# Kernel optimization log

Hardware: AMD Instinct MI355X
Metric: run time of the kernel (lower is better)

Reference implementation:

```python
import jax, jax.numpy as jnp
import numpy as np

B_COEF = 0.1          # position-offset scale 'b'
STRIDE = (1, 1)
PADDING = (1, 1)


def setup_inputs() -> dict:
    key = jax.random.key(0)
    k1, k2, k3 = jax.random.split(key, 3)
    x = jax.random.normal(k1, (16, 64, 128, 128), dtype=jnp.float32)
    kernel = jax.random.normal(k2, (128, 64, 3, 3), dtype=jnp.float32)
    bias = jax.random.normal(k3, (128,), dtype=jnp.float32)
    return {"x": x, "kernel": kernel, "bias": bias}


def _conv(inp, w):
    pads = [(PADDING[0], PADDING[0]), (PADDING[1], PADDING[1])]
    return jax.lax.conv_general_dilated(
        inp, w, window_strides=STRIDE, padding=pads,
        dimension_numbers=("NCHW", "OIHW", "NCHW"))


def reference(x, kernel, bias):
    # out[b,o,p] = sum_i x_unf[b,i,p] * (kernel_flat[o,i] + b*grid[p]) + bias[o]
    # = conv(x, kernel) + b*grid[p] * sum_i x_unf[b,i,p] + bias  (rank-1 separable)
    kh, kw = kernel.shape[2], kernel.shape[3]
    main = _conv(x, kernel)                                  # (B, O, Ho, Wo)
    H_out, W_out = main.shape[2], main.shape[3]

    # sum over in_channels and kernel window = ones-conv of channel-summed input
    ones_k = jnp.ones((1, 1, kh, kw), dtype=x.dtype)
    patch_sum = _conv(x.sum(axis=1, keepdims=True), ones_k)  # (B, 1, Ho, Wo)

    # Replicate torch meshgrid(arange(W_out), arange(H_out), indexing='ij')
    # -> flatten (W,H) row-major -> consumed as (H,W) row-major by the view.
    gx = jnp.arange(W_out)[:, None] + jnp.arange(H_out)[None, :]  # (Wo, Ho)
    grid2d = gx.reshape(-1).reshape(H_out, W_out).astype(x.dtype)  # (Ho, Wo)

    return main + B_COEF * grid2d * patch_sum + bias[None, :, None, None]
```

## Files before the change

### kernel.cpp

```cpp
#include <hip/hip_runtime.h>
#include <hip/hip_bf16.h>


typedef __attribute__((ext_vector_type(8))) short short8;
typedef __attribute__((ext_vector_type(4))) float f32x4;

#define B_COEF 0.1f
constexpr int CI = 64, CO = 128, H = 128, W = 128;
constexpr int XPAD = 72;

static __device__ inline short bf16s(float v) {
    __hip_bfloat16 b = __float2bfloat16(v);
    return *reinterpret_cast<short*>(&b);
}


__global__ __launch_bounds__(256)
void prep_x(const float* __restrict__ x, __hip_bfloat16* __restrict__ xt,
            float* __restrict__ S) {
    __shared__ float tile[64 * 129];
    __shared__ float ssum[256];
    const int h = blockIdx.x, b = blockIdx.y, tid = threadIdx.x;
    const int w = tid & 127, cip = tid >> 7;

    float sacc = 0.0f;
    for (int it = 0; it < 32; ++it) {
        int ci = it * 2 + cip;
        float v = x[(((size_t)b * CI + ci) * H + h) * W + w];
        tile[ci * 129 + w] = v;
        sacc += v;
    }
    ssum[tid] = sacc;
    __syncthreads();
    if (tid < 128)
        S[((size_t)b * H + h) * W + tid] = ssum[tid] + ssum[tid + 128];

    const int c8 = (tid & 7) * 8, wl = tid >> 3;
#pragma unroll
    for (int it = 0; it < 4; ++it) {
        int ww = wl + it * 32;
        short8 pk;
#pragma unroll
        for (int j = 0; j < 8; ++j)
            pk[j] = bf16s(tile[(c8 + j) * 129 + ww]);
        *(short8*)(xt + (((size_t)b * H + h) * W + ww) * CI + c8) = pk;
    }
}

__global__ void prep_wq(const float* __restrict__ wgt, __hip_bfloat16* __restrict__ wq) {
    int idx = blockIdx.x * 256 + threadIdx.x;
    if (idx < 9 * CO * CI) {
        int tap = idx >> 13;
        int rem = idx & 8191;
        int oc = rem >> 6, ci = rem & 63;
        int kc = ci >> 5, j = ci & 31;
        wq[(((tap * 2 + kc) * CO + oc) << 5) + j] =
            __float2bfloat16(wgt[(oc * CI + ci) * 9 + tap]);
    }
}

__global__ __launch_bounds__(256, 2)
void conv_main(const __hip_bfloat16* __restrict__ xt,
               const __hip_bfloat16* __restrict__ wq,
               const float* __restrict__ S,
               const float* __restrict__ bias,
               float* __restrict__ out) {
    __shared__ __hip_bfloat16 xrow[3][130 * XPAD];
    __shared__ float ssum[132];

    const int tid = threadIdx.x, h = blockIdx.x, b = blockIdx.y;
    const int lane = tid & 63, waveid = tid >> 6;
    const int lo16 = lane & 15, quad = lane >> 4;
    const int m0 = (waveid & 1) * 64, n0 = (waveid >> 1) * 64;

    const int c8 = (tid & 7) * 8, wl = tid >> 3;
#pragma unroll
    for (int r = 0; r < 3; ++r) {
        const int gh = h - 1 + r;
#pragma unroll
        for (int it = 0; it < 5; ++it) {
            int w = wl + it * 32;
            if (w < 130) {
                int gw = w - 1;
                short8 v = {0, 0, 0, 0, 0, 0, 0, 0};
                if (gh >= 0 && gh < H && gw >= 0 && gw < W)
                    v = *(const short8*)(xt + (((size_t)b * H + gh) * W + gw) * CI + c8);
                *(short8*)&xrow[r][w * XPAD + c8] = v;
            }
        }
    }
    if (tid < 130) {
        int gw = tid - 1;
        float s = 0.0f;
        if (gw >= 0 && gw < W) {
#pragma unroll
            for (int r = 0; r < 3; ++r) {
                int gh = h - 1 + r;
                if (gh >= 0 && gh < H) s += S[((size_t)b * H + gh) * W + gw];
            }
        }
        ssum[tid] = s;
    }
    __syncthreads();

    f32x4 acc[4][4] = {};

#pragma unroll
    for (int kh = 0; kh < 3; ++kh) {
#pragma unroll
        for (int kw = 0; kw < 3; ++kw) {
            const int tap = kh * 3 + kw;
            short8 bq[2][4];
#pragma unroll
            for (int kc = 0; kc < 2; ++kc)
#pragma unroll
                for (int ni = 0; ni < 4; ++ni)
                    bq[kc][ni] = *(const short8*)(
                        wq + (((tap * 2 + kc) * CO + n0 + ni * 16 + lo16) << 5) + quad * 8);
#pragma unroll
            for (int kc = 0; kc < 2; ++kc) {
                short8 af[4];
#pragma unroll
                for (int mi = 0; mi < 4; ++mi)
                    af[mi] = *(const short8*)
                        &xrow[kh][(m0 + mi * 16 + lo16 + kw) * XPAD + kc * 32 + quad * 8];
#pragma unroll
                for (int mi = 0; mi < 4; ++mi)
#pragma unroll
                    for (int ni = 0; ni < 4; ++ni)
                        acc[mi][ni] = __builtin_amdgcn_mfma_f32_16x16x32_bf16(
                            af[mi], bq[kc][ni], acc[mi][ni], 0, 0, 0);
            }
        }
    }

#pragma unroll
    for (int mi = 0; mi < 4; ++mi) {
        const int wbase = m0 + mi * 16 + quad * 4;
        float cs[6];
#pragma unroll
        for (int r = 0; r < 6; ++r) cs[r] = ssum[wbase + r];
        float ps[4], cf[4];
#pragma unroll
        for (int r = 0; r < 4; ++r) {
            ps[r] = cs[r] + cs[r + 1] + cs[r + 2];
            cf[r] = B_COEF * (float)(h + wbase + r);
        }
#pragma unroll
        for (int ni = 0; ni < 4; ++ni) {
            const int oc = n0 + ni * 16 + lo16;
            const float bv = bias[oc];
            f32x4 v = acc[mi][ni];
#pragma unroll
            for (int r = 0; r < 4; ++r) v[r] = v[r] + cf[r] * ps[r] + bv;
            *(f32x4*)(out + (((size_t)b * CO + oc) * H + h) * W + wbase) = v;
        }
    }
}


constexpr int WPAD = 72;

__global__ void prep_w_fb(const float* __restrict__ wgt, __hip_bfloat16* __restrict__ wt) {
    int idx = blockIdx.x * 256 + threadIdx.x;
    if (idx < 9 * CO * CI) {
        int tap = idx / (CO * CI);
        int rem = idx - tap * (CO * CI);
        int oc = rem >> 6, ci = rem & 63;
        wt[idx] = __float2bfloat16(wgt[(oc * CI + ci) * 9 + tap]);
    }
}

__global__ __launch_bounds__(256, 2)
void conv_fb(const float* __restrict__ x, const __hip_bfloat16* __restrict__ wt,
             const float* __restrict__ bias, float* __restrict__ out) {
    __shared__ __hip_bfloat16 xrow[130 * XPAD];
    __shared__ __hip_bfloat16 wlds[CO * WPAD];
    __shared__ float colsum[132];

    const int tid = threadIdx.x;
    const int h = blockIdx.x, b = blockIdx.y;
    const int lane = tid & 63, waveid = tid >> 6;
    const int lo16 = lane & 15, quad = lane >> 4;
    const int m0 = (waveid & 1) * 64, n0 = (waveid >> 1) * 64;

    f32x4 acc[4][4] = {};
    if (tid < 132) colsum[tid] = 0.0f;
    const float* xb = x + (size_t)b * CI * H * W;

    const int w16 = tid & 15, cipl = (tid >> 4) & 3, rest0 = tid >> 6;

    for (int kh = 0; kh < 3; ++kh) {
        const int gh = h - 1 + kh;
        __syncthreads();
        for (int it = 0; it < 18; ++it) {
            int rest = rest0 + it * 4;
            int whi = rest % 9, ciph = rest / 9;
            int w = whi * 16 + w16;
            int ci0 = (ciph * 4 + cipl) * 2;
            int gw = w - 1;
            float x0 = 0.0f, x1 = 0.0f;
            if (w < 130 && gw >= 0 && gw < W && gh >= 0 && gh < H) {
                const float* p = xb + (size_t)ci0 * (H * W) + gh * W + gw;
                x0 = p[0];
                x1 = p[H * W];
            }
            if (w < 130) {
                __hip_bfloat162 pk;
                pk.x = __float2bfloat16(x0);
                pk.y = __float2bfloat16(x1);
                *(__hip_bfloat162*)&xrow[w * XPAD + ci0] = pk;
            }
            float cs = x0 + x1;
            cs += __shfl_xor(cs, 16);
            cs += __shfl_xor(cs, 32);
            if (quad == 0 && w < 130) atomicAdd(&colsum[w], cs);
        }
        for (int kw = 0; kw < 3; ++kw) {
            __syncthreads();
            {
                const __hip_bfloat16* wtap = wt + (kh * 3 + kw) * (CO * CI);
#pragma unroll
                for (int it = 0; it < 4; ++it) {
                    int j = tid + it * 256;
                    int oc = j >> 3, ch = (j & 7) * 8;
                    short8 v = *(const short8*)(wtap + oc * CI + ch);
                    *(short8*)&wlds[oc * WPAD + ch] = v;
                }
            }
            __syncthreads();
#pragma unroll
            for (int kc = 0; kc < 2; ++kc) {
                const int krow = kc * 32 + quad * 8;
                short8 af[4], bf[4];
#pragma unroll
                for (int mi = 0; mi < 4; ++mi)
                    af[mi] = *(const short8*)&xrow[(m0 + mi * 16 + lo16 + kw) * XPAD + krow];
#pragma unroll
                for (int ni = 0; ni < 4; ++ni)
                    bf[ni] = *(const short8*)&wlds[(n0 + ni * 16 + lo16) * WPAD + krow];
#pragma unroll
                for (int mi = 0; mi < 4; ++mi)
#pragma unroll
                    for (int ni = 0; ni < 4; ++ni)
                        acc[mi][ni] = __builtin_amdgcn_mfma_f32_16x16x32_bf16(
                            af[mi], bf[ni], acc[mi][ni], 0, 0, 0);
            }
        }
    }
    __syncthreads();
#pragma unroll
    for (int mi = 0; mi < 4; ++mi) {
        const int wbase = m0 + mi * 16 + quad * 4;
        float cs[6];
#pragma unroll
        for (int r = 0; r < 6; ++r) cs[r] = colsum[wbase + r];
        float ps[4], cf[4];
#pragma unroll
        for (int r = 0; r < 4; ++r) {
            ps[r] = cs[r] + cs[r + 1] + cs[r + 2];
            cf[r] = B_COEF * (float)(h + wbase + r);
        }
#pragma unroll
        for (int ni = 0; ni < 4; ++ni) {
            const int oc = n0 + ni * 16 + lo16;
            const float bv = bias[oc];
            f32x4 v = acc[mi][ni];
#pragma unroll
            for (int r = 0; r < 4; ++r) v[r] = v[r] + cf[r] * ps[r] + bv;
            *(f32x4*)(out + (((size_t)b * CO + oc) * H + h) * W + wbase) = v;
        }
    }
}


extern "C" void kernel_launch(void* const* d_in, const int* in_sizes, int n_in,
                              void* d_out, int out_size, void* d_ws, size_t ws_size,
                              hipStream_t stream) {
    const float* x    = (const float*)d_in[0];
    const float* wgt  = (const float*)d_in[1];
    const float* bias = (const float*)d_in[2];
    float* out = (float*)d_out;

    const size_t XT_BYTES = (size_t)16 * H * W * CI * 2;
    const size_t S_BYTES  = (size_t)16 * H * W * 4;
    const size_t WQ_BYTES = (size_t)9 * 2 * CO * 32 * 2;

    if (ws_size >= XT_BYTES + S_BYTES + WQ_BYTES) {
        __hip_bfloat16* xt = (__hip_bfloat16*)d_ws;
        float* S           = (float*)((char*)d_ws + XT_BYTES);
        __hip_bfloat16* wq = (__hip_bfloat16*)((char*)d_ws + XT_BYTES + S_BYTES);
        prep_x<<<dim3(H, 16), dim3(256), 0, stream>>>(x, xt, S);
        prep_wq<<<dim3(288), dim3(256), 0, stream>>>(wgt, wq);
        conv_main<<<dim3(H, 16), dim3(256), 0, stream>>>(xt, wq, S, bias, out);
    } else {
        __hip_bfloat16* wt = (__hip_bfloat16*)d_ws;
        prep_w_fb<<<dim3(288), dim3(256), 0, stream>>>(wgt, wt);
        conv_fb<<<dim3(H, 16), dim3(256), 0, stream>>>(x, wt, bias, out);
    }
}
```

Before: 249.3 us.

## Compute two output rows per conv block and vectorize prep_x transpose

conv_main now computes two output rows per block. It loads four input rows into shared memory and reuses each weight fragment across both rows, which halves the grid and the redundant halo-row and weight loads. prep_x now does 128-bit vector global loads, uses an XOR-swizzled shared tile to avoid bank conflicts, and reduces channel sums through eight partial buffers. Both kernels remap blockIdx to row indices, likely to spread work across XCDs or cache. The larger accumulator array doubles register pressure and may reduce occupancy or cause spills.

```diff
diff --git a/kernel.cpp b/kernel.cpp
--- a/kernel.cpp
+++ b/kernel.cpp
@@ -18,31 +18,43 @@
 __global__ __launch_bounds__(256)
 void prep_x(const float* __restrict__ x, __hip_bfloat16* __restrict__ xt,
             float* __restrict__ S) {
-    __shared__ float tile[64 * 129];
-    __shared__ float ssum[256];
-    const int h = blockIdx.x, b = blockIdx.y, tid = threadIdx.x;
-    const int w = tid & 127, cip = tid >> 7;
-
-    float sacc = 0.0f;
-    for (int it = 0; it < 32; ++it) {
-        int ci = it * 2 + cip;
-        float v = x[(((size_t)b * CI + ci) * H + h) * W + w];
-        tile[ci * 129 + w] = v;
-        sacc += v;
-    }
-    ssum[tid] = sacc;
+    __shared__ float tile[64 * 132];
+    __shared__ float psum[8 * 128];
+    const int bx = blockIdx.x, b = blockIdx.y, tid = threadIdx.x;
+    const int h = ((bx & 7) << 4) | (bx >> 3);
+    const int q = tid & 31, cbase = tid >> 5;
+
+    const float* xp = x + (((size_t)b * CI + cbase * 8) * H + h) * W + q * 4;
+    f32x4 v[8];
+#pragma unroll
+    for (int it = 0; it < 8; ++it)
+        v[it] = *(const f32x4*)(xp + (size_t)it * H * W);
+
+    const int cw = 4 * (q ^ cbase);
+    f32x4 sacc = v[0];
+#pragma unroll
+    for (int it = 0; it < 8; ++it) {
+        *(f32x4*)&tile[(cbase * 8 + it) * 132 + cw] = v[it];
+        if (it) sacc += v[it];
+    }
+    *(f32x4*)&psum[cbase * 128 + 4 * q] = sacc;
     __syncthreads();
-    if (tid < 128)
-        S[((size_t)b * H + h) * W + tid] = ssum[tid] + ssum[tid + 128];
-
-    const int c8 = (tid & 7) * 8, wl = tid >> 3;
+
+    if (tid < 128) {
+        float s = 0.0f;
+#pragma unroll
+        for (int g = 0; g < 8; ++g) s += psum[g * 128 + tid];
+        S[((size_t)b * H + h) * W + tid] = s;
+    }
+
+    const int c8 = (tid & 7) * 8, wl = tid >> 3, sw = 4 * (tid & 7);
 #pragma unroll
     for (int it = 0; it < 4; ++it) {
         int ww = wl + it * 32;
         short8 pk;
 #pragma unroll
         for (int j = 0; j < 8; ++j)
-            pk[j] = bf16s(tile[(c8 + j) * 129 + ww]);
+            pk[j] = bf16s(tile[(c8 + j) * 132 + (ww ^ sw)]);
         *(short8*)(xt + (((size_t)b * H + h) * W + ww) * CI + c8) = pk;
     }
 }
@@ -65,18 +77,20 @@
                const float* __restrict__ S,
                const float* __restrict__ bias,
                float* __restrict__ out) {
-    __shared__ __hip_bfloat16 xrow[3][130 * XPAD];
-    __shared__ float ssum[132];
-
-    const int tid = threadIdx.x, h = blockIdx.x, b = blockIdx.y;
+    __shared__ __hip_bfloat16 xrow[4][130 * XPAD];
+    __shared__ float ssum[2][132];
+
+    const int tid = threadIdx.x, bx = blockIdx.x, b = blockIdx.y;
+    const int strip = ((bx & 7) << 3) | (bx >> 3);
+    const int h0 = strip * 2;
     const int lane = tid & 63, waveid = tid >> 6;
     const int lo16 = lane & 15, quad = lane >> 4;
     const int m0 = (waveid & 1) * 64, n0 = (waveid >> 1) * 64;
 
     const int c8 = (tid & 7) * 8, wl = tid >> 3;
 #pragma unroll
-    for (int r = 0; r < 3; ++r) {
-        const int gh = h - 1 + r;
+    for (int r = 0; r < 4; ++r) {
+        const int gh = h0 - 1 + r;
 #pragma unroll
         for (int it = 0; it < 5; ++it) {
             int w = wl + it * 32;
@@ -91,19 +105,20 @@
     }
     if (tid < 130) {
         int gw = tid - 1;
-        float s = 0.0f;
+        float s4[4] = {0.0f, 0.0f, 0.0f, 0.0f};
         if (gw >= 0 && gw < W) {
 #pragma unroll
-            for (int r = 0; r < 3; ++r) {
-                int gh = h - 1 + r;
-                if (gh >= 0 && gh < H) s += S[((size_t)b * H + gh) * W + gw];
-            }
-        }
-        ssum[tid] = s;
+            for (int r = 0; r < 4; ++r) {
+                int gh = h0 - 1 + r;
+                if (gh >= 0 && gh < H) s4[r] = S[((size_t)b * H + gh) * W + gw];
+            }
+        }
+        ssum[0][tid] = s4[0] + s4[1] + s4[2];
+        ssum[1][tid] = s4[1] + s4[2] + s4[3];
     }
     __syncthreads();
 
-    f32x4 acc[4][4] = {};
+    f32x4 acc[2][4][4] = {};
 
 #pragma unroll
     for (int kh = 0; kh < 3; ++kh) {
@@ -118,42 +133,49 @@
                     bq[kc][ni] = *(const short8*)(
                         wq + (((tap * 2 + kc) * CO + n0 + ni * 16 + lo16) << 5) + quad * 8);
 #pragma unroll
-            for (int kc = 0; kc < 2; ++kc) {
-                short8 af[4];
-#pragma unroll
-                for (int mi = 0; mi < 4; ++mi)
-                    af[mi] = *(const short8*)
-                        &xrow[kh][(m0 + mi * 16 + lo16 + kw) * XPAD + kc * 32 + quad * 8];
-#pragma unroll
-                for (int mi = 0; mi < 4; ++mi)
-#pragma unroll
-                    for (int ni = 0; ni < 4; ++ni)
-                        acc[mi][ni] = __builtin_amdgcn_mfma_f32_16x16x32_bf16(
-                            af[mi], bq[kc][ni], acc[mi][ni], 0, 0, 0);
-            }
-        }
-    }
-
-#pragma unroll
-    for (int mi = 0; mi < 4; ++mi) {
-        const int wbase = m0 + mi * 16 + quad * 4;
-        float cs[6];
-#pragma unroll
-        for (int r = 0; r < 6; ++r) cs[r] = ssum[wbase + r];
-        float ps[4], cf[4];
-#pragma unroll
-        for (int r = 0; r < 4; ++r) {
-            ps[r] = cs[r] + cs[r + 1] + cs[r + 2];
-            cf[r] = B_COEF * (float)(h + wbase + r);
-        }
-#pragma unroll
-        for (int ni = 0; ni < 4; ++ni) {
-            const int oc = n0 + ni * 16 + lo16;
-            const float bv = bias[oc];
-            f32x4 v = acc[mi][ni];
-#pragma unroll
-            for (int r = 0; r < 4; ++r) v[r] = v[r] + cf[r] * ps[r] + bv;
-            *(f32x4*)(out + (((size_t)b * CO + oc) * H + h) * W + wbase) = v;
+            for (int r = 0; r < 2; ++r) {
+#pragma unroll
+                for (int kc = 0; kc < 2; ++kc) {
+                    short8 af[4];
+#pragma unroll
+                    for (int mi = 0; mi < 4; ++mi)
+                        af[mi] = *(const short8*)
+                            &xrow[kh + r][(m0 + mi * 16 + lo16 + kw) * XPAD + kc * 32 + quad * 8];
+#pragma unroll
+                    for (int mi = 0; mi < 4; ++mi)
+#pragma unroll
+                        for (int ni = 0; ni < 4; ++ni)
+                            acc[r][mi][ni] = __builtin_amdgcn_mfma_f32_16x16x32_bf16(
+                                af[mi], bq[kc][ni], acc[r][mi][ni], 0, 0, 0);
+                }
+            }
+        }
+    }
+
+#pragma unroll
+    for (int r = 0; r < 2; ++r) {
+        const int h = h0 + r;
+#pragma unroll
+        for (int mi = 0; mi < 4; ++mi) {
+            const int wbase = m0 + mi * 16 + quad * 4;
+            float cs[6];
+#pragma unroll
+            for (int t = 0; t < 6; ++t) cs[t] = ssum[r][wbase + t];
+            float ps[4], cf[4];
+#pragma unroll
+            for (int t = 0; t < 4; ++t) {
+                ps[t] = cs[t] + cs[t + 1] + cs[t + 2];
+                cf[t] = B_COEF * (float)(h + wbase + t);
+            }
+#pragma unroll
+            for (int ni = 0; ni < 4; ++ni) {
+                const int oc = n0 + ni * 16 + lo16;
+                const float bv = bias[oc];
+                f32x4 vv = acc[r][mi][ni];
+#pragma unroll
+                for (int t = 0; t < 4; ++t) vv[t] = vv[t] + cf[t] * ps[t] + bv;
+                *(f32x4*)(out + (((size_t)b * CO + oc) * H + h) * W + wbase) = vv;
+            }
         }
     }
 }
@@ -292,7 +314,7 @@
         __hip_bfloat16* wq = (__hip_bfloat16*)((char*)d_ws + XT_BYTES + S_BYTES);
         prep_x<<<dim3(H, 16), dim3(256), 0, stream>>>(x, xt, S);
         prep_wq<<<dim3(288), dim3(256), 0, stream>>>(wgt, wq);
-        conv_main<<<dim3(H, 16), dim3(256), 0, stream>>>(xt, wq, S, bias, out);
+        conv_main<<<dim3(H / 2, 16), dim3(256), 0, stream>>>(xt, wq, S, bias, out);
     } else {
         __hip_bfloat16* wt = (__hip_bfloat16*)d_ws;
         prep_w_fb<<<dim3(288), dim3(256), 0, stream>>>(wgt, wt);
```

Result: slower. 257.9 us (+3.4%).

## Fuse input transpose and channel-sum into conv kernel with swizzled LDS

Applied to the files above, without the earlier changes.

Removes the separate prep_x pass that wrote a bf16 NHWC copy of x and a channel-sum buffer. The conv kernel now reads fp32 x directly for its three input rows, converts it to bf16 into an XOR-swizzled LDS tile, and computes the channel sums in place. It also remaps blockIdx to interleave rows, raises the occupancy hint to 3 blocks, and sets wave priority around the MFMA loop. The cost is that each input row is now read and converted three times, once by each neighbouring output-row block, in exchange for dropping an intermediate global write and read.

```diff
diff --git a/kernel.cpp b/kernel.cpp
--- a/kernel.cpp
+++ b/kernel.cpp
@@ -14,38 +14,6 @@
     return *reinterpret_cast<short*>(&b);
 }
 
-
-__global__ __launch_bounds__(256)
-void prep_x(const float* __restrict__ x, __hip_bfloat16* __restrict__ xt,
-            float* __restrict__ S) {
-    __shared__ float tile[64 * 129];
-    __shared__ float ssum[256];
-    const int h = blockIdx.x, b = blockIdx.y, tid = threadIdx.x;
-    const int w = tid & 127, cip = tid >> 7;
-
-    float sacc = 0.0f;
-    for (int it = 0; it < 32; ++it) {
-        int ci = it * 2 + cip;
-        float v = x[(((size_t)b * CI + ci) * H + h) * W + w];
-        tile[ci * 129 + w] = v;
-        sacc += v;
-    }
-    ssum[tid] = sacc;
-    __syncthreads();
-    if (tid < 128)
-        S[((size_t)b * H + h) * W + tid] = ssum[tid] + ssum[tid + 128];
-
-    const int c8 = (tid & 7) * 8, wl = tid >> 3;
-#pragma unroll
-    for (int it = 0; it < 4; ++it) {
-        int ww = wl + it * 32;
-        short8 pk;
-#pragma unroll
-        for (int j = 0; j < 8; ++j)
-            pk[j] = bf16s(tile[(c8 + j) * 129 + ww]);
-        *(short8*)(xt + (((size_t)b * H + h) * W + ww) * CI + c8) = pk;
-    }
-}
 
 __global__ void prep_wq(const float* __restrict__ wgt, __hip_bfloat16* __restrict__ wq) {
     int idx = blockIdx.x * 256 + threadIdx.x;
@@ -59,52 +27,63 @@
     }
 }
 
-__global__ __launch_bounds__(256, 2)
-void conv_main(const __hip_bfloat16* __restrict__ xt,
-               const __hip_bfloat16* __restrict__ wq,
-               const float* __restrict__ S,
-               const float* __restrict__ bias,
-               float* __restrict__ out) {
-    __shared__ __hip_bfloat16 xrow[3][130 * XPAD];
-    __shared__ float ssum[132];
-
-    const int tid = threadIdx.x, h = blockIdx.x, b = blockIdx.y;
+__global__ __launch_bounds__(256, 3)
+void conv_fused(const float* __restrict__ x,
+                const __hip_bfloat16* __restrict__ wq,
+                const float* __restrict__ bias,
+                float* __restrict__ out) {
+    __shared__ __hip_bfloat16 xrow[3][130 * 64];
+    __shared__ float psum[256];
+    __shared__ float ssumL[130];
+
+    const int tid = threadIdx.x, bx = blockIdx.x, b = blockIdx.y;
+    const int h = ((bx & 7) << 4) | (bx >> 3);
     const int lane = tid & 63, waveid = tid >> 6;
     const int lo16 = lane & 15, quad = lane >> 4;
     const int m0 = (waveid & 1) * 64, n0 = (waveid >> 1) * 64;
 
-    const int c8 = (tid & 7) * 8, wl = tid >> 3;
-#pragma unroll
-    for (int r = 0; r < 3; ++r) {
-        const int gh = h - 1 + r;
-#pragma unroll
-        for (int it = 0; it < 5; ++it) {
-            int w = wl + it * 32;
-            if (w < 130) {
-                int gw = w - 1;
-                short8 v = {0, 0, 0, 0, 0, 0, 0, 0};
-                if (gh >= 0 && gh < H && gw >= 0 && gw < W)
-                    v = *(const short8*)(xt + (((size_t)b * H + gh) * W + gw) * CI + c8);
-                *(short8*)&xrow[r][w * XPAD + c8] = v;
-            }
-        }
-    }
-    if (tid < 130) {
-        int gw = tid - 1;
-        float s = 0.0f;
-        if (gw >= 0 && gw < W) {
-#pragma unroll
-            for (int r = 0; r < 3; ++r) {
-                int gh = h - 1 + r;
-                if (gh >= 0 && gh < H) s += S[((size_t)b * H + gh) * W + gw];
-            }
-        }
-        ssum[tid] = s;
-    }
+    if (tid < 48) {
+        const int r = tid >> 4, s = ((tid >> 3) & 1) ? 129 : 0, u = tid & 7;
+        short8 z = {0, 0, 0, 0, 0, 0, 0, 0};
+        *(short8*)&xrow[r][s * 64 + ((u ^ (s & 7)) * 8)] = z;
+    }
+
+    const int wl = tid & 127, cg0 = tid >> 7;
+    const int wslot = wl + 1, wsw = wslot & 7;
+    float sacc = 0.0f;
+    const float* xb = x + (size_t)b * CI * H * W + wl;
+#pragma unroll
+    for (int p = 0; p < 4; ++p) {
+        const int cg = cg0 + 2 * p;
+#pragma unroll
+        for (int r = 0; r < 3; ++r) {
+            const int gh = h - 1 + r;
+            short8 pk = {0, 0, 0, 0, 0, 0, 0, 0};
+            if (gh >= 0 && gh < H) {
+                const float* px = xb + ((size_t)(cg * 8) * H + gh) * W;
+                float v[8];
+#pragma unroll
+                for (int j = 0; j < 8; ++j) v[j] = px[(size_t)j * H * W];
+#pragma unroll
+                for (int j = 0; j < 8; ++j) {
+                    pk[j] = bf16s(v[j]);
+                    sacc += v[j];
+                }
+            }
+            *(short8*)&xrow[r][wslot * 64 + ((cg ^ wsw) * 8)] = pk;
+        }
+    }
+    psum[tid] = sacc;
     __syncthreads();
 
+    if (tid < 128) ssumL[tid + 1] = psum[tid] + psum[tid + 128];
+    if (tid == 128) ssumL[0] = 0.0f;
+    if (tid == 129) ssumL[129] = 0.0f;
+    __syncthreads();
+
     f32x4 acc[4][4] = {};
 
+    __builtin_amdgcn_s_setprio(1);
 #pragma unroll
     for (int kh = 0; kh < 3; ++kh) {
 #pragma unroll
@@ -121,9 +100,11 @@
             for (int kc = 0; kc < 2; ++kc) {
                 short8 af[4];
 #pragma unroll
-                for (int mi = 0; mi < 4; ++mi)
+                for (int mi = 0; mi < 4; ++mi) {
+                    const int row = m0 + mi * 16 + lo16 + kw;
                     af[mi] = *(const short8*)
-                        &xrow[kh][(m0 + mi * 16 + lo16 + kw) * XPAD + kc * 32 + quad * 8];
+                        &xrow[kh][row * 64 + (((kc * 4 + quad) ^ (row & 7)) * 8)];
+                }
 #pragma unroll
                 for (int mi = 0; mi < 4; ++mi)
 #pragma unroll
@@ -133,18 +114,19 @@
             }
         }
     }
+    __builtin_amdgcn_s_setprio(0);
 
 #pragma unroll
     for (int mi = 0; mi < 4; ++mi) {
         const int wbase = m0 + mi * 16 + quad * 4;
         float cs[6];
 #pragma unroll
-        for (int r = 0; r < 6; ++r) cs[r] = ssum[wbase + r];
+        for (int t = 0; t < 6; ++t) cs[t] = ssumL[wbase + t];
         float ps[4], cf[4];
 #pragma unroll
-        for (int r = 0; r < 4; ++r) {
-            ps[r] = cs[r] + cs[r + 1] + cs[r + 2];
-            cf[r] = B_COEF * (float)(h + wbase + r);
+        for (int t = 0; t < 4; ++t) {
+            ps[t] = cs[t] + cs[t + 1] + cs[t + 2];
+            cf[t] = B_COEF * (float)(h + wbase + t);
         }
 #pragma unroll
         for (int ni = 0; ni < 4; ++ni) {
@@ -152,7 +134,7 @@
             const float bv = bias[oc];
             f32x4 v = acc[mi][ni];
 #pragma unroll
-            for (int r = 0; r < 4; ++r) v[r] = v[r] + cf[r] * ps[r] + bv;
+            for (int t = 0; t < 4; ++t) v[t] = v[t] + cf[t] * ps[t] + bv;
             *(f32x4*)(out + (((size_t)b * CO + oc) * H + h) * W + wbase) = v;
         }
     }
@@ -282,17 +264,12 @@
     const float* bias = (const float*)d_in[2];
     float* out = (float*)d_out;
 
-    const size_t XT_BYTES = (size_t)16 * H * W * CI * 2;
-    const size_t S_BYTES  = (size_t)16 * H * W * 4;
     const size_t WQ_BYTES = (size_t)9 * 2 * CO * 32 * 2;
 
-    if (ws_size >= XT_BYTES + S_BYTES + WQ_BYTES) {
-        __hip_bfloat16* xt = (__hip_bfloat16*)d_ws;
-        float* S           = (float*)((char*)d_ws + XT_BYTES);
-        __hip_bfloat16* wq = (__hip_bfloat16*)((char*)d_ws + XT_BYTES + S_BYTES);
-        prep_x<<<dim3(H, 16), dim3(256), 0, stream>>>(x, xt, S);
+    if (ws_size >= WQ_BYTES) {
+        __hip_bfloat16* wq = (__hip_bfloat16*)d_ws;
         prep_wq<<<dim3(288), dim3(256), 0, stream>>>(wgt, wq);
-        conv_main<<<dim3(H, 16), dim3(256), 0, stream>>>(xt, wq, S, bias, out);
+        conv_fused<<<dim3(H, 16), dim3(256), 0, stream>>>(x, wq, bias, out);
     } else {
         __hip_bfloat16* wt = (__hip_bfloat16*)d_ws;
         prep_w_fb<<<dim3(288), dim3(256), 0, stream>>>(wgt, wt);
```

After: 229.9 us. 7.8% less time.
